# Kernel tuning notes

Hardware: AMD Instinct MI355X
Metric: run time of the kernel (lower is better)

The kernel has to match this reference:

```python
import jax, jax.numpy as jnp
import numpy as np

H = 50  # hidden_layer_size

def _lstm_layer(x, Wih, Whh, bih, bhh):
    # x: [B, T, D_in]; Wih: [4H, D_in]; Whh: [4H, H]; biases: [4H]
    # Precompute input contribution to all gates for every timestep.
    xg = jnp.einsum('btd,gd->btg', x, Wih) + bih + bhh  # [B, T, 4H]
    xg = jnp.transpose(xg, (1, 0, 2))                   # [T, B, 4H] for scan
    B = x.shape[0]
    h0 = jnp.zeros((B, H), x.dtype)
    c0 = jnp.zeros((B, H), x.dtype)

    def step(carry, xt):
        h, c = carry
        g = xt + h @ Whh.T                              # [B, 4H]
        i, f, gg, o = jnp.split(g, 4, axis=-1)          # PyTorch gate order i,f,g,o
        i = jax.nn.sigmoid(i)
        f = jax.nn.sigmoid(f)
        gg = jnp.tanh(gg)
        o = jax.nn.sigmoid(o)
        c = f * c + i * gg
        h = o * jnp.tanh(c)
        return (h, c), h

    (_, _), hs = jax.lax.scan(step, (h0, c0), xg)       # hs: [T, B, H]
    return jnp.transpose(hs, (1, 0, 2))                 # [B, T, H]


def setup_inputs() -> dict:
    key = jax.random.key(0)
    ks = jax.random.split(key, 11)
    B, T, D = 4096, 512, 1
    s = 1.0 / np.sqrt(H)  # PyTorch LSTM init scale
    inp = {
        'x': jax.random.normal(ks[0], (B, T, D), jnp.float32),
        'W_ih0': jax.random.uniform(ks[1], (4 * H, D), jnp.float32, -s, s),
        'W_hh0': jax.random.uniform(ks[2], (4 * H, H), jnp.float32, -s, s),
        'b_ih0': jax.random.uniform(ks[3], (4 * H,), jnp.float32, -s, s),
        'b_hh0': jax.random.uniform(ks[4], (4 * H,), jnp.float32, -s, s),
        'W_ih1': jax.random.uniform(ks[5], (4 * H, H), jnp.float32, -s, s),
        'W_hh1': jax.random.uniform(ks[6], (4 * H, H), jnp.float32, -s, s),
        'b_ih1': jax.random.uniform(ks[7], (4 * H,), jnp.float32, -s, s),
        'b_hh1': jax.random.uniform(ks[8], (4 * H,), jnp.float32, -s, s),
        'fc_W': jax.random.uniform(ks[9], (1, H), jnp.float32, -s, s),
        'fc_b': jax.random.uniform(ks[10], (1,), jnp.float32, -s, s),
    }
    return inp


def reference(x, W_ih0, W_hh0, b_ih0, b_hh0, W_ih1, W_hh1, b_ih1, b_hh1, fc_W, fc_b):
    h1 = _lstm_layer(x, W_ih0, W_hh0, b_ih0, b_hh0)     # [B, T, H]
    h2 = _lstm_layer(h1, W_ih1, W_hh1, b_ih1, b_hh1)    # [B, T, H]
    last = h2[:, -1, :]                                 # [B, H]
    return last @ fc_W.T + fc_b                         # [B, 1]
```

## Files before the change

### kernel.cpp

```cpp
#include <hip/hip_runtime.h>


typedef __attribute__((ext_vector_type(8))) _Float16 half8;
typedef __attribute__((ext_vector_type(4))) float f32x4;

#define LOG2E 1.44269504088896340736f

__device__ __forceinline__ float rcp_(float x) { return __builtin_amdgcn_rcpf(x); }
__device__ __forceinline__ float exp2_(float x) { return __builtin_amdgcn_exp2f(x); }
__device__ __forceinline__ float sigm(float x) {
  return rcp_(1.f + exp2_(-LOG2E * x));
}
__device__ __forceinline__ float tanh_(float x) {
  return 1.f - 2.f * rcp_(1.f + exp2_(2.f * LOG2E * x));
}
__device__ __forceinline__ f32x4 mfma16(half8 a, half8 b, f32x4 c) {
  return __builtin_amdgcn_mfma_f32_16x16x32_f16(a, b, c, 0, 0, 0);
}

union ABu { struct { uint2 a, b; } u; half8 v; };
__device__ __forceinline__ half8 rdfrag(const _Float16* p0, const _Float16* p1) {
  ABu t;
  t.u.a = *(const uint2*)p0;
  t.u.b = *(const uint2*)p1;
  return t.v;
}

__device__ __forceinline__ void loadW(const float* __restrict__ W, int n,
                                      int gate, int kbase, int lg,
                                      half8& h8, half8& l8) {
#pragma unroll
  for (int e = 0; e < 8; ++e) {
    const int k = kbase + 16 * (e >> 2) + 4 * lg + (e & 3);
    const bool v = (n < 50) && (k < 50);
    const float w = v ? W[(gate * 50 + n) * 50 + k] : 0.f;
    const _Float16 hi = (_Float16)w;
    h8[e] = hi;
    l8[e] = (_Float16)(w - (float)hi);
  }
}

#define GATES(X) X(0) X(1) X(2) X(3)

__global__ __launch_bounds__(512) void lstm2_kernel(
    const float* __restrict__ x,
    const float* __restrict__ Wih0, const float* __restrict__ Whh0,
    const float* __restrict__ bih0, const float* __restrict__ bhh0,
    const float* __restrict__ Wih1, const float* __restrict__ Whh1,
    const float* __restrict__ bih1, const float* __restrict__ bhh1,
    const float* __restrict__ fcW, const float* __restrict__ fcb,
    float* __restrict__ out) {
  const int tid = threadIdx.x;
  const int lane = tid & 63;
  const int wv = tid >> 6;
  const int wg = wv & 3;
  const bool isL1 = wv >= 4;
  const int lg = lane >> 4;
  const int l15 = lane & 15;
  const int bbase = blockIdx.x * 16;

  __shared__ _Float16 H0[2][1024], H1[2][1024];
  __shared__ float xs2[64][16];
  __shared__ float ldspad[18688];

  ((volatile float*)ldspad)[tid] = 0.f;

  for (int i = tid; i < 1024; i += 512) {
    ((unsigned int*)H0)[i] = 0u;
    ((unsigned int*)H1)[i] = 0u;
  }

  const int lane4 = lane * 4;
  const int u = 16 * wg + l15;
  const bool uv = (u < 50);
  const int woff = ((u >> 5) << 9) + (((u >> 4) & 1) << 8) +
                   (((u >> 2) & 3) << 6) + ((4 * lg) << 2) + (u & 3);

#define STAGE(c)                                                        \
  {                                                                     \
    const int b_ = tid >> 4, fg_ = tid & 15;                            \
    const float4 v_ = *(const float4*)&x[(size_t)(bbase + b_) * 512 +   \
                                         (c) * 64 + 4 * fg_];           \
    xs2[4 * fg_ + 0][b_] = v_.x; xs2[4 * fg_ + 1][b_] = v_.y;           \
    xs2[4 * fg_ + 2][b_] = v_.z; xs2[4 * fg_ + 3][b_] = v_.w;           \
  }

  if (!isL1) {
#define DECL0(G) half8 W0h_##G, W0l_##G, W1h_##G, W1l_##G;  \
    float bi_##G = 0.f, wx_##G = 0.f;
    GATES(DECL0)
#define LOAD0(G)                                              \
    { loadW(Whh0, u, G, 0, lg, W0h_##G, W0l_##G);             \
      loadW(Whh0, u, G, 32, lg, W1h_##G, W1l_##G);            \
      if (uv) {                                               \
        bi_##G = bih0[G * 50 + u] + bhh0[G * 50 + u];         \
        wx_##G = Wih0[G * 50 + u];                            \
      } }
    GATES(LOAD0)
    float cc0 = 0.f, cc1 = 0.f, cc2 = 0.f, cc3 = 0.f;

#define MM0(G, ACC)                                           \
    ACC = mfma16(f0, W0h_##G, ACC);                           \
    ACC = mfma16(f0, W0l_##G, ACC);                           \
    ACC = mfma16(f1, W1h_##G, ACC);                           \
    ACC = mfma16(f1, W1l_##G, ACC);
#define FIN0(r, WP)                                           \
    { const float i_ = sigm(ai[r]), ff = sigm(af[r]);         \
      const float g_ = tanh_(ag[r]), o_ = sigm(ao[r]);        \
      cc##r = ff * cc##r + i_ * g_;                           \
      H0[WP][woff + 4 * (r)] = (_Float16)(o_ * tanh_(cc##r)); }

#define L0STEP(RP, WP, tm)                                                  \
    { const half8 f0 = rdfrag(&H0[RP][lane4], &H0[RP][lane4 + 256]);        \
      const half8 f1 = rdfrag(&H0[RP][512 + lane4], &H0[RP][768 + lane4]);  \
      const float4 xv = *(const float4*)&xs2[tm][4 * lg];                   \
      f32x4 ai = {fmaf(xv.x, wx_0, bi_0), fmaf(xv.y, wx_0, bi_0),           \
                  fmaf(xv.z, wx_0, bi_0), fmaf(xv.w, wx_0, bi_0)};          \
      f32x4 af = {fmaf(xv.x, wx_1, bi_1), fmaf(xv.y, wx_1, bi_1),           \
                  fmaf(xv.z, wx_1, bi_1), fmaf(xv.w, wx_1, bi_1)};          \
      f32x4 ag = {fmaf(xv.x, wx_2, bi_2), fmaf(xv.y, wx_2, bi_2),           \
                  fmaf(xv.z, wx_2, bi_2), fmaf(xv.w, wx_2, bi_2)};          \
      f32x4 ao = {fmaf(xv.x, wx_3, bi_3), fmaf(xv.y, wx_3, bi_3),           \
                  fmaf(xv.z, wx_3, bi_3), fmaf(xv.w, wx_3, bi_3)};          \
      MM0(0, ai) MM0(1, af) MM0(2, ag) MM0(3, ao)                           \
      FIN0(0, WP) FIN0(1, WP) FIN0(2, WP) FIN0(3, WP) }

    STAGE(0) __syncthreads();
    L0STEP(1, 0, 0) __syncthreads();
    for (int it = 0; it < 255; ++it) {
      const int todd = 2 * it + 1;
      L0STEP(0, 1, (todd & 63)) __syncthreads();
      const int tev = todd + 1;
      if ((tev & 63) == 0) { STAGE(tev >> 6) __syncthreads(); }
      L0STEP(1, 0, (tev & 63)) __syncthreads();
    }
    L0STEP(0, 1, 63) __syncthreads();
    __syncthreads();
  } else {
#define DECL1(G) half8 I0h_##G, I0l_##G, I1h_##G, I1l_##G,    \
        R0h_##G, R0l_##G, R1h_##G, R1l_##G;                   \
    float bi_##G = 0.f;
    GATES(DECL1)
#define LOAD1(G)                                              \
    { loadW(Wih1, u, G, 0, lg, I0h_##G, I0l_##G);             \
      loadW(Wih1, u, G, 32, lg, I1h_##G, I1l_##G);            \
      loadW(Whh1, u, G, 0, lg, R0h_##G, R0l_##G);             \
      loadW(Whh1, u, G, 32, lg, R1h_##G, R1l_##G);            \
      if (uv) bi_##G = bih1[G * 50 + u] + bhh1[G * 50 + u]; }
    GATES(LOAD1)
    float cc0 = 0.f, cc1 = 0.f, cc2 = 0.f, cc3 = 0.f;

#define MM1(G, ACC)                                           \
    ACC = mfma16(f0, I0h_##G, ACC);                           \
    ACC = mfma16(f0, I0l_##G, ACC);                           \
    ACC = mfma16(f1, I1h_##G, ACC);                           \
    ACC = mfma16(f1, I1l_##G, ACC);                           \
    ACC = mfma16(g0, R0h_##G, ACC);                           \
    ACC = mfma16(g0, R0l_##G, ACC);                           \
    ACC = mfma16(g1, R1h_##G, ACC);                           \
    ACC = mfma16(g1, R1l_##G, ACC);
#define FIN1(r, W1)                                           \
    { const float i_ = sigm(ai[r]), ff = sigm(af[r]);         \
      const float g_ = tanh_(ag[r]), o_ = sigm(ao[r]);        \
      cc##r = ff * cc##r + i_ * g_;                           \
      H1[W1][woff + 4 * (r)] = (_Float16)(o_ * tanh_(cc##r)); }

#define L1STEP(P0, R1, W1)                                                  \
    { const half8 f0 = rdfrag(&H0[P0][lane4], &H0[P0][lane4 + 256]);        \
      const half8 f1 = rdfrag(&H0[P0][512 + lane4], &H0[P0][768 + lane4]);  \
      const half8 g0 = rdfrag(&H1[R1][lane4], &H1[R1][lane4 + 256]);        \
      const half8 g1 = rdfrag(&H1[R1][512 + lane4], &H1[R1][768 + lane4]);  \
      f32x4 ai = {bi_0, bi_0, bi_0, bi_0};                                  \
      f32x4 af = {bi_1, bi_1, bi_1, bi_1};                                  \
      f32x4 ag = {bi_2, bi_2, bi_2, bi_2};                                  \
      f32x4 ao = {bi_3, bi_3, bi_3, bi_3};                                  \
      MM1(0, ai) MM1(1, af) MM1(2, ag) MM1(3, ao)                           \
      FIN1(0, W1) FIN1(1, W1) FIN1(2, W1) FIN1(3, W1) }

    __syncthreads(); __syncthreads();
    for (int it = 0; it < 255; ++it) {
      L1STEP(0, 1, 0) __syncthreads();
      if (((2 * it + 2) & 63) == 0) __syncthreads();
      L1STEP(1, 0, 1) __syncthreads();
    }
    L1STEP(0, 1, 0) __syncthreads();
    L1STEP(1, 0, 1) __syncthreads();
  }

  if (tid < 16) {
    float s = fcb[0];
    for (int j = 0; j < 50; ++j) {
      const int idx = ((j >> 5) << 9) + (((j >> 4) & 1) << 8) +
                      (((j >> 2) & 3) << 6) + (tid << 2) + (j & 3);
      s += fcW[j] * (float)H1[1][idx];
    }
    out[bbase + tid] = s;
  }
}

extern "C" void kernel_launch(void* const* d_in, const int* in_sizes, int n_in,
                              void* d_out, int out_size, void* d_ws, size_t ws_size,
                              hipStream_t stream) {
  const float* x    = (const float*)d_in[0];
  const float* Wih0 = (const float*)d_in[1];
  const float* Whh0 = (const float*)d_in[2];
  const float* bih0 = (const float*)d_in[3];
  const float* bhh0 = (const float*)d_in[4];
  const float* Wih1 = (const float*)d_in[5];
  const float* Whh1 = (const float*)d_in[6];
  const float* bih1 = (const float*)d_in[7];
  const float* bhh1 = (const float*)d_in[8];
  const float* fcW  = (const float*)d_in[9];
  const float* fcb  = (const float*)d_in[10];
  float* out = (float*)d_out;

  const int B = out_size;
  const int blocks = B / 16;
  lstm2_kernel<<<dim3(blocks), dim3(512), 0, stream>>>(
      x, Wih0, Whh0, bih0, bhh0, Wih1, Whh1, bih1, bhh1, fcW, fcb, out);
}
```

Baseline: 480.0 us.

## Merge LSTM gate reciprocals and use single 16-byte LDS fragment reads

Rewrites the gate activation math so the i, f, g sigmoids/tanh share one reciprocal for the cell update and the output gate and cell tanh share a second, cutting per-element rcp count from six to two, with clamps to keep the products from overflowing. Also re-lays out the fp16 hidden-state buffers so each lane's MFMA A fragment is contiguous, replacing two 8-byte LDS reads with one 16-byte read per fragment. The clamps slightly change numerics at extreme activations, and the new interleaved layout alters the LDS bank pattern of the scattered fp16 writes.

```diff
diff --git a/kernel.cpp b/kernel.cpp
--- a/kernel.cpp
+++ b/kernel.cpp
@@ -8,21 +8,14 @@
 
 __device__ __forceinline__ float rcp_(float x) { return __builtin_amdgcn_rcpf(x); }
 __device__ __forceinline__ float exp2_(float x) { return __builtin_amdgcn_exp2f(x); }
-__device__ __forceinline__ float sigm(float x) {
-  return rcp_(1.f + exp2_(-LOG2E * x));
-}
-__device__ __forceinline__ float tanh_(float x) {
-  return 1.f - 2.f * rcp_(1.f + exp2_(2.f * LOG2E * x));
-}
 __device__ __forceinline__ f32x4 mfma16(half8 a, half8 b, f32x4 c) {
   return __builtin_amdgcn_mfma_f32_16x16x32_f16(a, b, c, 0, 0, 0);
 }
 
-union ABu { struct { uint2 a, b; } u; half8 v; };
-__device__ __forceinline__ half8 rdfrag(const _Float16* p0, const _Float16* p1) {
-  ABu t;
-  t.u.a = *(const uint2*)p0;
-  t.u.b = *(const uint2*)p1;
+union ABu16 { uint4 u; half8 v; };
+__device__ __forceinline__ half8 rdfrag(const _Float16* p) {
+  ABu16 t;
+  t.u = *(const uint4*)p;
   return t.v;
 }
 
@@ -41,6 +34,24 @@
 }
 
 #define GATES(X) X(0) X(1) X(2) X(3)
+
+#define FINX(r, PH, WPc)                                                 \
+  {                                                                      \
+    const float xi = fmaxf(ai[r], -20.f), xf = fmaxf(af[r], -20.f);      \
+    const float xg = fmaxf(ag[r], -20.f), xo = fmaxf(ao[r], -20.f);      \
+    const float ei = exp2_(-LOG2E * xi), ef = exp2_(-LOG2E * xf);        \
+    const float uu = exp2_(-2.f * LOG2E * xg), eo = exp2_(-LOG2E * xo);  \
+    const float pi = 1.f + ei, pf = 1.f + ef;                            \
+    const float pu = 1.f + uu, po = 1.f + eo;                            \
+    const float P = pi * pu;                                             \
+    const float R = rcp_(P * pf);                                        \
+    const float num = cc##r * P + (1.f - uu) * pf;                       \
+    cc##r = num * R;                                                     \
+    const float ct = fmaxf(cc##r, -10.f);                                \
+    const float v = exp2_(-2.f * LOG2E * ct);                            \
+    const float R2 = rcp_(po * (1.f + v));                               \
+    PH[WPc][woff + 8 * (r)] = (_Float16)((1.f - v) * R2);                \
+  }
 
 __global__ __launch_bounds__(512) void lstm2_kernel(
     const float* __restrict__ x,
@@ -59,7 +70,7 @@
   const int l15 = lane & 15;
   const int bbase = blockIdx.x * 16;
 
-  __shared__ _Float16 H0[2][1024], H1[2][1024];
+  __shared__ __align__(16) _Float16 H0[2][1024], H1[2][1024];
   __shared__ float xs2[64][16];
   __shared__ float ldspad[18688];
 
@@ -70,11 +81,11 @@
     ((unsigned int*)H1)[i] = 0u;
   }
 
-  const int lane4 = lane * 4;
+  const int lane8 = lane * 8;
   const int u = 16 * wg + l15;
   const bool uv = (u < 50);
-  const int woff = ((u >> 5) << 9) + (((u >> 4) & 1) << 8) +
-                   (((u >> 2) & 3) << 6) + ((4 * lg) << 2) + (u & 3);
+  const int woff = ((u >> 5) << 9) + (((u >> 2) & 3) << 7) + ((4 * lg) << 3) +
+                   (((u >> 4) & 1) << 2) + (u & 3);
 
 #define STAGE(c)                                                        \
   {                                                                     \
@@ -104,15 +115,10 @@
     ACC = mfma16(f0, W0l_##G, ACC);                           \
     ACC = mfma16(f1, W1h_##G, ACC);                           \
     ACC = mfma16(f1, W1l_##G, ACC);
-#define FIN0(r, WP)                                           \
-    { const float i_ = sigm(ai[r]), ff = sigm(af[r]);         \
-      const float g_ = tanh_(ag[r]), o_ = sigm(ao[r]);        \
-      cc##r = ff * cc##r + i_ * g_;                           \
-      H0[WP][woff + 4 * (r)] = (_Float16)(o_ * tanh_(cc##r)); }
 
 #define L0STEP(RP, WP, tm)                                                  \
-    { const half8 f0 = rdfrag(&H0[RP][lane4], &H0[RP][lane4 + 256]);        \
-      const half8 f1 = rdfrag(&H0[RP][512 + lane4], &H0[RP][768 + lane4]);  \
+    { const half8 f0 = rdfrag(&H0[RP][lane8]);                              \
+      const half8 f1 = rdfrag(&H0[RP][512 + lane8]);                        \
       const float4 xv = *(const float4*)&xs2[tm][4 * lg];                   \
       f32x4 ai = {fmaf(xv.x, wx_0, bi_0), fmaf(xv.y, wx_0, bi_0),           \
                   fmaf(xv.z, wx_0, bi_0), fmaf(xv.w, wx_0, bi_0)};          \
@@ -123,7 +129,7 @@
       f32x4 ao = {fmaf(xv.x, wx_3, bi_3), fmaf(xv.y, wx_3, bi_3),           \
                   fmaf(xv.z, wx_3, bi_3), fmaf(xv.w, wx_3, bi_3)};          \
       MM0(0, ai) MM0(1, af) MM0(2, ag) MM0(3, ao)                           \
-      FIN0(0, WP) FIN0(1, WP) FIN0(2, WP) FIN0(3, WP) }
+      FINX(0, H0, WP) FINX(1, H0, WP) FINX(2, H0, WP) FINX(3, H0, WP) }
 
     STAGE(0) __syncthreads();
     L0STEP(1, 0, 0) __syncthreads();
@@ -159,23 +165,18 @@
     ACC = mfma16(g0, R0l_##G, ACC);                           \
     ACC = mfma16(g1, R1h_##G, ACC);                           \
     ACC = mfma16(g1, R1l_##G, ACC);
-#define FIN1(r, W1)                                           \
-    { const float i_ = sigm(ai[r]), ff = sigm(af[r]);         \
-      const float g_ = tanh_(ag[r]), o_ = sigm(ao[r]);        \
-      cc##r = ff * cc##r + i_ * g_;                           \
-      H1[W1][woff + 4 * (r)] = (_Float16)(o_ * tanh_(cc##r)); }
 
 #define L1STEP(P0, R1, W1)                                                  \
-    { const half8 f0 = rdfrag(&H0[P0][lane4], &H0[P0][lane4 + 256]);        \
-      const half8 f1 = rdfrag(&H0[P0][512 + lane4], &H0[P0][768 + lane4]);  \
-      const half8 g0 = rdfrag(&H1[R1][lane4], &H1[R1][lane4 + 256]);        \
-      const half8 g1 = rdfrag(&H1[R1][512 + lane4], &H1[R1][768 + lane4]);  \
+    { const half8 f0 = rdfrag(&H0[P0][lane8]);                              \
+      const half8 f1 = rdfrag(&H0[P0][512 + lane8]);                        \
+      const half8 g0 = rdfrag(&H1[R1][lane8]);                              \
+      const half8 g1 = rdfrag(&H1[R1][512 + lane8]);                        \
       f32x4 ai = {bi_0, bi_0, bi_0, bi_0};                                  \
       f32x4 af = {bi_1, bi_1, bi_1, bi_1};                                  \
       f32x4 ag = {bi_2, bi_2, bi_2, bi_2};                                  \
       f32x4 ao = {bi_3, bi_3, bi_3, bi_3};                                  \
       MM1(0, ai) MM1(1, af) MM1(2, ag) MM1(3, ao)                           \
-      FIN1(0, W1) FIN1(1, W1) FIN1(2, W1) FIN1(3, W1) }
+      FINX(0, H1, W1) FINX(1, H1, W1) FINX(2, H1, W1) FINX(3, H1, W1) }
 
     __syncthreads(); __syncthreads();
     for (int it = 0; it < 255; ++it) {
@@ -190,8 +191,8 @@
   if (tid < 16) {
     float s = fcb[0];
     for (int j = 0; j < 50; ++j) {
-      const int idx = ((j >> 5) << 9) + (((j >> 4) & 1) << 8) +
-                      (((j >> 2) & 3) << 6) + (tid << 2) + (j & 3);
+      const int idx = ((j >> 5) << 9) + (((j >> 2) & 3) << 7) + (tid << 3) +
+                      (((j >> 4) & 1) << 2) + (j & 3);
       s += fcW[j] * (float)H1[1][idx];
     }
     out[bbase + tid] = s;
```

Measured after the change: 485.1 us. Within noise of the previous version (+1.1%).
